# Kernel tuning notes

Measured on AMD Instinct MI355X. Metric: run time of the kernel, lower is better.

The kernel has to match this reference:

```python
import jax, jax.numpy as jnp
import numpy as np

WINDOW = (2, 6, 12)  # (Wz, Wy, Wx)
HEADS = 6


def _position_index(window):
    Wz, Wy, Wx = window
    cz, cy, cx = np.arange(Wz), np.arange(Wy), np.arange(Wx)
    coords = np.stack(np.meshgrid(cz, cy, cx, indexing='ij'))  # [3, Wz, Wy, Wx]
    cf = coords.reshape(3, -1)                                  # [3, N]
    rel = cf[:, :, None] - cf[:, None, :]                       # [3, N, N]
    rel = rel.transpose(1, 2, 0).astype(np.int64)               # [N, N, 3]
    rel[:, :, 0] += Wz - 1
    rel[:, :, 1] += Wy - 1
    rel[:, :, 2] += Wx - 1
    rel[:, :, 0] *= 2 * Wy - 1
    return jnp.asarray(rel.sum(-1).reshape(-1))                 # [N*N]


def setup_inputs() -> dict:
    key = jax.random.key(0)
    ks = jax.random.split(key, 7)
    dim, N, B_, nW = 192, 144, 1024, 512
    table_rows = (2 * WINDOW[2] - 1) * (2 * WINDOW[1] - 1) * (2 * WINDOW[0] - 1)  # 759
    return {
        'x': jax.random.normal(ks[0], (B_, N, dim), jnp.float32),
        'mask': jax.random.normal(ks[1], (nW, N, N), jnp.float32),
        'w_qkv': jax.random.normal(ks[2], (dim, 3 * dim), jnp.float32) * 0.02,
        'b_qkv': jax.random.normal(ks[3], (3 * dim,), jnp.float32) * 0.02,
        'w_o': jax.random.normal(ks[4], (dim, dim), jnp.float32) * 0.02,
        'b_o': jax.random.normal(ks[5], (dim,), jnp.float32) * 0.02,
        'bias_table': jax.random.normal(ks[6], (table_rows, 1, HEADS), jnp.float32) * 0.02,
    }


def reference(x, mask, w_qkv, b_qkv, w_o, b_o, bias_table):
    B_, N, dim = x.shape
    H = HEADS
    hd = dim // H
    scale = hd ** -0.5

    qkv = x @ w_qkv + b_qkv                              # [B_, N, 3*dim]
    qkv = qkv.reshape(B_, N, 3, H, hd).transpose(2, 0, 3, 1, 4)
    q, k, v = qkv[0], qkv[1], qkv[2]                     # [B_, H, N, hd]

    attn = jnp.einsum('bhnd,bhmd->bhnm', q * scale, k)   # [B_, H, N, N]

    pos_idx = _position_index(WINDOW)                    # [N*N] int constant
    bias = bias_table[pos_idx].reshape(N, N, H).transpose(2, 0, 1)  # [H, N, N]
    attn = attn + bias[None]

    nW = mask.shape[0]
    attn = attn.reshape(B_ // nW, nW, H, N, N) + mask[None, :, None]
    attn = jax.nn.softmax(attn.reshape(B_, H, N, N), axis=-1)

    out = jnp.einsum('bhnm,bhmd->bhnd', attn, v)         # [B_, H, N, hd]
    out = out.transpose(0, 2, 1, 3).reshape(B_, N, dim)
    return out @ w_o + b_o
```

## Files before the change

### kernel.cpp

```cpp
#include <hip/hip_runtime.h>

typedef __attribute__((ext_vector_type(4))) float  f32x4;
typedef __attribute__((ext_vector_type(4))) float  float4v;
typedef __attribute__((ext_vector_type(4))) short  short4v;
typedef __attribute__((ext_vector_type(8))) short  short8v;
typedef __attribute__((ext_vector_type(2))) unsigned uint2v;
typedef __attribute__((ext_vector_type(8))) __bf16 bf16x8;

union Frag { short4v h[2]; short8v s8; unsigned u[4]; };
union BF4  { uint2v u2; short4v s4; };

__device__ __forceinline__ short f2bf(float f) {
  unsigned u = __builtin_bit_cast(unsigned, f);
  u = (u + 0x7fffu + ((u >> 16) & 1u)) >> 16;
  return (short)u;
}

__device__ __forceinline__ unsigned cvt_pk_bf16(float a, float b) {
  unsigned r;
  asm("v_cvt_pk_bf16_f32 %0, %1, %2" : "=v"(r) : "v"(a), "v"(b));
  return r;
}
__device__ __forceinline__ short4v f4_to_bf4(float4v v) {
  BF4 r;
  r.u2 = uint2v{ cvt_pk_bf16(v[0], v[1]), cvt_pk_bf16(v[2], v[3]) };
  return r.s4;
}

__device__ __forceinline__ f32x4 mfma_bf16(const Frag& a, const Frag& b, f32x4 c) {
  return __builtin_amdgcn_mfma_f32_16x16x32_bf16(
      __builtin_bit_cast(bf16x8, a.s8), __builtin_bit_cast(bf16x8, b.s8), c, 0, 0, 0);
}

__device__ __forceinline__ int poscode(int i) {
  int z = (i >= 72) ? 1 : 0;
  int rem = i - 72 * z;
  int y = rem / 12;
  return 11 * z + y + (rem - 12 * y);
}

__device__ __forceinline__ int kperm(int r) {
  return (r & 16) ? (((r - 16) >> 2) * 8 + 4 + (r & 3)) : ((r >> 2) * 8 + (r & 3));
}

__global__ __launch_bounds__(256) void k_transpose_w(
    const float* __restrict__ w_qkv, const float* __restrict__ w_o,
    short* __restrict__ wtq, short* __restrict__ wto) {
  int idx = blockIdx.x * 256 + threadIdx.x;
  if (idx < 110592) {
    int k = idx / 576, c = idx % 576;
    int kp = (k & ~31) + kperm(k & 31);
    wtq[c * 192 + kp] = f2bf(w_qkv[idx]);
  } else {
    int j = idx - 110592;
    int k = j / 192, c = j % 192;
    wto[c * 192 + k] = f2bf(w_o[j]);
  }
}

__global__ __launch_bounds__(256) void k_bias(
    const float* __restrict__ btab, float* __restrict__ bias6) {
  int idx = blockIdx.x * 256 + threadIdx.x;
  if (idx >= 124416) return;
  int h = idx / 20736, r = idx % 20736, m = r / 144, n = r % 144;
  bias6[idx] = btab[(poscode(m) - poscode(n) + 27) * 6 + h];
}

__global__ __launch_bounds__(256, 2) void k_qkv(
    const float* __restrict__ x, const float* __restrict__ bqkv,
    const short* __restrict__ wtq, short* __restrict__ qkv) {
  __shared__ short a_lds[128][200];
  __shared__ short bT[288][40];
  const int tid = threadIdx.x;
  const int lane = tid & 63, wv = tid >> 6;
  const int l15 = lane & 15, lg = lane >> 4;

  const int did = blockIdx.x;
  const int vid = (did & 7) * 288 + (did >> 3);
  const int row0 = (vid >> 1) * 128;
  const int col0 = (vid & 1) * 288;

#pragma unroll
  for (int i = 0; i < 24; ++i) {
    int flat = tid + 256 * i;
    int r = flat / 48, c4 = flat % 48;
    float4v xv = *(const float4v*)&x[(size_t)(row0 + r) * 192 + c4 * 4];
    int k = c4 * 4, rr = k & 31;
    int pos = (k & ~31) + ((rr & 16) ? (((rr - 16) >> 2) * 8 + 4) : ((rr >> 2) * 8));
    *(short4v*)&a_lds[r][pos] = f4_to_bf4(xv);
  }

  f32x4 acc[2][18];
#pragma unroll
  for (int ai = 0; ai < 2; ++ai)
#pragma unroll
    for (int i = 0; i < 18; ++i) acc[ai][i] = f32x4{0.f, 0.f, 0.f, 0.f};

  for (int kc = 0; kc < 6; ++kc) {
    __syncthreads();
#pragma unroll
    for (int i = 0; i < 5; ++i) {
      int flat = tid + 256 * i;
      if (flat < 1152) {
        int c = flat >> 2, j = flat & 3;
        *(short8v*)&bT[c][j * 8] =
            *(const short8v*)&wtq[(col0 + c) * 192 + kc * 32 + j * 8];
      }
    }
    __syncthreads();
    Frag a0, a1;
    a0.s8 = *(const short8v*)&a_lds[wv * 32 + l15][kc * 32 + lg * 8];
    a1.s8 = *(const short8v*)&a_lds[wv * 32 + 16 + l15][kc * 32 + lg * 8];
#pragma unroll
    for (int cf = 0; cf < 18; ++cf) {
      Frag bw;
      bw.s8 = *(const short8v*)&bT[cf * 16 + l15][lg * 8];
      acc[0][cf] = mfma_bf16(bw, a0, acc[0][cf]);
      acc[1][cf] = mfma_bf16(bw, a1, acc[1][cf]);
    }
  }

#pragma unroll
  for (int ai = 0; ai < 2; ++ai) {
    const int g = row0 + wv * 32 + ai * 16 + l15;
    const int b_ = g / 144, n = g - b_ * 144;
#pragma unroll
    for (int cf = 0; cf < 18; ++cf) {
      int c0 = col0 + cf * 16 + lg * 4;
      int part = c0 / 192, rem = c0 % 192;
      int h = rem >> 5, d0 = rem & 31;
      int q4 = d0 >> 2;
      int dd0 = (part == 2) ? d0 : ((q4 < 4) ? q4 * 8 : (q4 - 4) * 8 + 4);
      float4v bias4 = *(const float4v*)&bqkv[c0];
      float scale = (part == 0) ? 0.17677669529663687f : 1.0f;
      float4v t = (acc[ai][cf] + bias4) * scale;
      *(short4v*)&qkv[(size_t)((part * 1024 + b_) * 6 + h) * 4608 + n * 32 + dd0] =
          f4_to_bf4(t);
    }
  }
}

__global__ __launch_bounds__(512, 4) void k_attn(
    const short* __restrict__ qkv, const float* __restrict__ mask,
    const float* __restrict__ bias6, float* __restrict__ out) {
  __shared__ short k_l[3][144][40];
  __shared__ short vt[3][32][168];
  const int tid = threadIdx.x;
  const int lane = tid & 63, wv = tid >> 6;
  const int l15 = lane & 15, lg = lane >> 4;

  const int did = blockIdx.x;
  const int vid = (did & 7) * 256 + (did >> 3);
  const int wm = vid >> 2, r4 = vid & 3;
  const int b = wm + (r4 >> 1) * 512;
  const int h0 = (r4 & 1) * 3;

  const size_t kbase = (size_t)((1024 + b) * 6 + h0) * 4608;
#pragma unroll
  for (int i = 0; i < 4; ++i) {
    int flat = tid + 512 * i;
    if (flat < 1728) {
      int h = flat / 576, r = flat % 576;
      int n = r >> 2, j8 = (r & 3) * 8;
      *(short8v*)&k_l[h][n][j8] =
          *(const short8v*)&qkv[kbase + (size_t)h * 4608 + n * 32 + j8];
    }
  }
#pragma unroll
  for (int i = 0; i < 3; ++i) {
    int flat = tid + 512 * i;
    int h = flat / 512, r = flat & 511;
    int d = r >> 4, jj = r & 15;
    vt[h][d][128 + (jj >> 2) * 8 + 4 + (jj & 3)] = 0;
  }
  const size_t vbase = (size_t)((2048 + b) * 6 + h0) * 4608;
#pragma unroll
  for (int i = 0; i < 7; ++i) {
    int flat = tid + 512 * i;
    if (flat < 3456) {
      int h = flat / 1152, r = flat % 1152;
      int n = r >> 3, d4 = (r & 7) * 4;
      short4v vv = *(const short4v*)&qkv[vbase + (size_t)h * 4608 + n * 32 + d4];
      int np = (n & ~31) + kperm(n & 31);
      vt[h][d4 + 0][np] = vv[0];
      vt[h][d4 + 1][np] = vv[1];
      vt[h][d4 + 2][np] = vv[2];
      vt[h][d4 + 3][np] = vv[3];
    }
  }
  __syncthreads();

  const float* maskw = &mask[(size_t)wm * 20736];
  const size_t qb = (size_t)(b * 6 + h0) * 4608;

  f32x4 mrow[9];
  int q = 0;
  for (int unit = 0; unit < 4; ++unit) {
    int t, hl;
    if (unit < 3) { t = wv; hl = unit; }
    else { if (wv >= 3) break; t = 8; hl = wv; }
    if (unit == 0 || unit == 3) {
      q = t * 16 + l15;
#pragma unroll
      for (int cf = 0; cf < 9; ++cf)
        mrow[cf] = *(const float4v*)&maskw[q * 144 + cf * 16 + lg * 4];
    }

    Frag aq;
    aq.s8 = *(const short8v*)&qkv[qb + (size_t)hl * 4608 + q * 32 + lg * 8];

    f32x4 s[9];
#pragma unroll
    for (int cf = 0; cf < 9; ++cf) {
      Frag bk;
      bk.s8 = *(const short8v*)&k_l[hl][cf * 16 + l15][lg * 8];
      s[cf] = mfma_bf16(bk, aq, f32x4{0.f, 0.f, 0.f, 0.f});
    }
    const float* brow = &bias6[(size_t)((h0 + hl) * 144 + q) * 144];
#pragma unroll
    for (int cf = 0; cf < 9; ++cf) {
      float4v bv = *(const float4v*)&brow[cf * 16 + lg * 4];
      s[cf] += mrow[cf] + bv;
    }

    float mx = s[0][0];
#pragma unroll
    for (int cf = 0; cf < 9; ++cf)
#pragma unroll
      for (int reg = 0; reg < 4; ++reg) mx = fmaxf(mx, s[cf][reg]);
    mx = fmaxf(mx, __shfl_xor(mx, 16, 64));
    mx = fmaxf(mx, __shfl_xor(mx, 32, 64));
    float sum = 0.f;
#pragma unroll
    for (int cf = 0; cf < 9; ++cf)
#pragma unroll
      for (int reg = 0; reg < 4; ++reg) {
        float e = __expf(s[cf][reg] - mx);
        s[cf][reg] = e;
        sum += e;
      }
    sum += __shfl_xor(sum, 16, 64);
    sum += __shfl_xor(sum, 32, 64);
    const float rinv = 1.0f / sum;

    f32x4 o0 = {0.f, 0.f, 0.f, 0.f}, o1 = {0.f, 0.f, 0.f, 0.f};
#pragma unroll
    for (int kc = 0; kc < 5; ++kc) {
      Frag p, b0, b1;
      p.u[0] = cvt_pk_bf16(s[2 * kc][0], s[2 * kc][1]);
      p.u[1] = cvt_pk_bf16(s[2 * kc][2], s[2 * kc][3]);
      if (kc < 4) {
        p.u[2] = cvt_pk_bf16(s[2 * kc + 1][0], s[2 * kc + 1][1]);
        p.u[3] = cvt_pk_bf16(s[2 * kc + 1][2], s[2 * kc + 1][3]);
      } else {
        p.u[2] = 0; p.u[3] = 0;
      }
      b0.s8 = *(const short8v*)&vt[hl][l15][kc * 32 + lg * 8];
      b1.s8 = *(const short8v*)&vt[hl][16 + l15][kc * 32 + lg * 8];
      o0 = mfma_bf16(b0, p, o0);
      o1 = mfma_bf16(b1, p, o1);
    }
    o0 *= rinv;
    o1 *= rinv;
    const size_t base = (size_t)(b * 144 + q) * 192 + (h0 + hl) * 32;
    *(float4v*)&out[base + lg * 4]      = o0;
    *(float4v*)&out[base + 16 + lg * 4] = o1;
  }
}

__global__ __launch_bounds__(256, 2) void k_oproj(
    float* __restrict__ io, const float* __restrict__ bo,
    const short* __restrict__ wto) {
  __shared__ short a_lds[64][200];
  __shared__ short bT[192][40];
  const int tid = threadIdx.x;
  const int lane = tid & 63, wv = tid >> 6;
  const int l15 = lane & 15, lg = lane >> 4;
  const int row0 = blockIdx.x * 64;

#pragma unroll
  for (int i = 0; i < 12; ++i) {
    int flat = tid + 256 * i;
    int r = flat / 48, c4 = flat % 48;
    float4v xv = *(const float4v*)&io[(size_t)(row0 + r) * 192 + c4 * 4];
    *(short4v*)&a_lds[r][c4 * 4] = f4_to_bf4(xv);
  }

  f32x4 acc[12];
#pragma unroll
  for (int i = 0; i < 12; ++i) acc[i] = f32x4{0.f, 0.f, 0.f, 0.f};

  for (int kc = 0; kc < 6; ++kc) {
    __syncthreads();
#pragma unroll
    for (int i = 0; i < 6; ++i) {
      int flat = tid + 256 * i;
      int c = flat >> 3, kk = (flat & 7) << 2;
      *(short4v*)&bT[c][kk] = *(const short4v*)&wto[c * 192 + kc * 32 + kk];
    }
    __syncthreads();
    Frag a;
    a.h[0] = *(const short4v*)&a_lds[wv * 16 + l15][kc * 32 + lg * 4];
    a.h[1] = *(const short4v*)&a_lds[wv * 16 + l15][kc * 32 + lg * 4 + 16];
#pragma unroll
    for (int cf = 0; cf < 12; ++cf) {
      Frag bw;
      bw.h[0] = *(const short4v*)&bT[cf * 16 + l15][lg * 4];
      bw.h[1] = *(const short4v*)&bT[cf * 16 + l15][lg * 4 + 16];
      acc[cf] = mfma_bf16(bw, a, acc[cf]);
    }
  }

  const int g = row0 + wv * 16 + l15;
#pragma unroll
  for (int cf = 0; cf < 12; ++cf) {
    int c0 = cf * 16 + lg * 4;
    float4v bias4 = *(const float4v*)&bo[c0];
    *(float4v*)&io[(size_t)g * 192 + c0] = acc[cf] + bias4;
  }
}

extern "C" void kernel_launch(void* const* d_in, const int* in_sizes, int n_in,
                              void* d_out, int out_size, void* d_ws, size_t ws_size,
                              hipStream_t stream) {
  const float* x    = (const float*)d_in[0];
  const float* mask = (const float*)d_in[1];
  const float* wqkv = (const float*)d_in[2];
  const float* bqkv = (const float*)d_in[3];
  const float* wo   = (const float*)d_in[4];
  const float* bo   = (const float*)d_in[5];
  const float* btab = (const float*)d_in[6];
  float* out = (float*)d_out;

  short* wtq   = (short*)d_ws;
  short* wto   = wtq + 110592;
  short* qkv   = wto + 36864;
  float* bias6 = (float*)(qkv + 84934656);

  k_transpose_w<<<576, 256, 0, stream>>>(wqkv, wo, wtq, wto);
  k_bias<<<486, 256, 0, stream>>>(btab, bias6);
  k_qkv<<<2304, 256, 0, stream>>>(x, bqkv, wtq, qkv);
  k_attn<<<2048, 512, 0, stream>>>(qkv, mask, bias6, out);
  k_oproj<<<2304, 256, 0, stream>>>(out, bo, wto);
}
```

Before: 312.3 us.

## Retile QKV GEMM to full-width 64-row blocks with register-prefetched weights

The QKV projection kernel now gives each block 64 rows and all 576 output columns, so x is converted once per row and the column split is gone. The next weight k-slice is loaded into registers while the current one is multiplied, which overlaps global loads with MFMA work and removes one barrier per step. The attention kernel's launch bound drops from 4 to 2 blocks per multiprocessor. This trades fewer wave-level A-fragment reuses (one 16-row fragment per wave instead of two) and a larger LDS footprint and register count for less redundant loading. The blocks-per-SM change on the attention kernel gives the compiler more registers but may reduce occupancy.

```diff
diff --git a/kernel.cpp b/kernel.cpp
--- a/kernel.cpp
+++ b/kernel.cpp
@@ -69,19 +69,22 @@
 __global__ __launch_bounds__(256, 2) void k_qkv(
     const float* __restrict__ x, const float* __restrict__ bqkv,
     const short* __restrict__ wtq, short* __restrict__ qkv) {
-  __shared__ short a_lds[128][200];
-  __shared__ short bT[288][40];
+  __shared__ short a_lds[64][200];
+  __shared__ short bT[576][40];
   const int tid = threadIdx.x;
   const int lane = tid & 63, wv = tid >> 6;
   const int l15 = lane & 15, lg = lane >> 4;
-
-  const int did = blockIdx.x;
-  const int vid = (did & 7) * 288 + (did >> 3);
-  const int row0 = (vid >> 1) * 128;
-  const int col0 = (vid & 1) * 288;
-
-#pragma unroll
-  for (int i = 0; i < 24; ++i) {
+  const int row0 = blockIdx.x * 64;
+  const int bc0 = tid >> 2;
+  const int bj8 = (tid & 3) * 8;
+
+  short8v bpre[9];
+#pragma unroll
+  for (int i = 0; i < 9; ++i)
+    bpre[i] = *(const short8v*)&wtq[(bc0 + 64 * i) * 192 + bj8];
+
+#pragma unroll
+  for (int i = 0; i < 12; ++i) {
     int flat = tid + 256 * i;
     int r = flat / 48, c4 = flat % 48;
     float4v xv = *(const float4v*)&x[(size_t)(row0 + r) * 192 + c4 * 4];
@@ -89,58 +92,56 @@
     int pos = (k & ~31) + ((rr & 16) ? (((rr - 16) >> 2) * 8 + 4) : ((rr >> 2) * 8));
     *(short4v*)&a_lds[r][pos] = f4_to_bf4(xv);
   }
-
-  f32x4 acc[2][18];
-#pragma unroll
-  for (int ai = 0; ai < 2; ++ai)
-#pragma unroll
-    for (int i = 0; i < 18; ++i) acc[ai][i] = f32x4{0.f, 0.f, 0.f, 0.f};
+#pragma unroll
+  for (int i = 0; i < 9; ++i)
+    *(short8v*)&bT[bc0 + 64 * i][bj8] = bpre[i];
+  __syncthreads();
+
+  f32x4 acc[36];
+#pragma unroll
+  for (int i = 0; i < 36; ++i) acc[i] = f32x4{0.f, 0.f, 0.f, 0.f};
 
   for (int kc = 0; kc < 6; ++kc) {
-    __syncthreads();
-#pragma unroll
-    for (int i = 0; i < 5; ++i) {
-      int flat = tid + 256 * i;
-      if (flat < 1152) {
-        int c = flat >> 2, j = flat & 3;
-        *(short8v*)&bT[c][j * 8] =
-            *(const short8v*)&wtq[(col0 + c) * 192 + kc * 32 + j * 8];
-      }
-    }
-    __syncthreads();
-    Frag a0, a1;
-    a0.s8 = *(const short8v*)&a_lds[wv * 32 + l15][kc * 32 + lg * 8];
-    a1.s8 = *(const short8v*)&a_lds[wv * 32 + 16 + l15][kc * 32 + lg * 8];
-#pragma unroll
-    for (int cf = 0; cf < 18; ++cf) {
+    if (kc < 5) {
+#pragma unroll
+      for (int i = 0; i < 9; ++i)
+        bpre[i] = *(const short8v*)&wtq[(bc0 + 64 * i) * 192 + (kc + 1) * 32 + bj8];
+    }
+    Frag a;
+    a.s8 = *(const short8v*)&a_lds[wv * 16 + l15][kc * 32 + lg * 8];
+#pragma unroll
+    for (int cf = 0; cf < 36; ++cf) {
       Frag bw;
       bw.s8 = *(const short8v*)&bT[cf * 16 + l15][lg * 8];
-      acc[0][cf] = mfma_bf16(bw, a0, acc[0][cf]);
-      acc[1][cf] = mfma_bf16(bw, a1, acc[1][cf]);
-    }
-  }
-
-#pragma unroll
-  for (int ai = 0; ai < 2; ++ai) {
-    const int g = row0 + wv * 32 + ai * 16 + l15;
-    const int b_ = g / 144, n = g - b_ * 144;
-#pragma unroll
-    for (int cf = 0; cf < 18; ++cf) {
-      int c0 = col0 + cf * 16 + lg * 4;
-      int part = c0 / 192, rem = c0 % 192;
-      int h = rem >> 5, d0 = rem & 31;
-      int q4 = d0 >> 2;
-      int dd0 = (part == 2) ? d0 : ((q4 < 4) ? q4 * 8 : (q4 - 4) * 8 + 4);
-      float4v bias4 = *(const float4v*)&bqkv[c0];
-      float scale = (part == 0) ? 0.17677669529663687f : 1.0f;
-      float4v t = (acc[ai][cf] + bias4) * scale;
-      *(short4v*)&qkv[(size_t)((part * 1024 + b_) * 6 + h) * 4608 + n * 32 + dd0] =
-          f4_to_bf4(t);
-    }
-  }
-}
-
-__global__ __launch_bounds__(512, 4) void k_attn(
+      acc[cf] = mfma_bf16(bw, a, acc[cf]);
+    }
+    __syncthreads();
+    if (kc < 5) {
+#pragma unroll
+      for (int i = 0; i < 9; ++i)
+        *(short8v*)&bT[bc0 + 64 * i][bj8] = bpre[i];
+      __syncthreads();
+    }
+  }
+
+  const int g = row0 + wv * 16 + l15;
+  const int b_ = g / 144, n = g - b_ * 144;
+#pragma unroll
+  for (int cf = 0; cf < 36; ++cf) {
+    int c0 = cf * 16 + lg * 4;
+    int part = c0 / 192, rem = c0 % 192;
+    int h = rem >> 5, d0 = rem & 31;
+    int q4 = d0 >> 2;
+    int dd0 = (part == 2) ? d0 : ((q4 < 4) ? q4 * 8 : (q4 - 4) * 8 + 4);
+    float4v bias4 = *(const float4v*)&bqkv[c0];
+    float scale = (part == 0) ? 0.17677669529663687f : 1.0f;
+    float4v t = (acc[cf] + bias4) * scale;
+    *(short4v*)&qkv[(size_t)((part * 1024 + b_) * 6 + h) * 4608 + n * 32 + dd0] =
+        f4_to_bf4(t);
+  }
+}
+
+__global__ __launch_bounds__(512, 2) void k_attn(
     const short* __restrict__ qkv, const float* __restrict__ mask,
     const float* __restrict__ bias6, float* __restrict__ out) {
   __shared__ short k_l[3][144][40];
```

After: 283.5 us. 1.1x faster.

## Fuse QKV projection into attention kernel, one block per window

Applied to the files above, without the earlier changes.

Merges the QKV projection GEMM and the attention kernel into one kernel. Each 576-thread block handles one window with all six heads: each wave computes Q/K/V for its 16 rows straight from x, keeps Q in registers and writes K and the transposed V into LDS. This removes the write and re-read of the large bf16 qkv intermediate in global memory and one kernel launch. In exchange, weight fragments are read from global/L2 with no LDS staging, LDS use per block doubles, and register pressure is high (x fragments plus six Q fragments), which may lower occupancy.

```diff
diff --git a/kernel.cpp b/kernel.cpp
--- a/kernel.cpp
+++ b/kernel.cpp
@@ -49,8 +49,7 @@
   int idx = blockIdx.x * 256 + threadIdx.x;
   if (idx < 110592) {
     int k = idx / 576, c = idx % 576;
-    int kp = (k & ~31) + kperm(k & 31);
-    wtq[c * 192 + kp] = f2bf(w_qkv[idx]);
+    wtq[c * 192 + (k & ~31) + kperm(k & 31)] = f2bf(w_qkv[idx]);
   } else {
     int j = idx - 110592;
     int k = j / 192, c = j % 192;
@@ -66,157 +65,95 @@
   bias6[idx] = btab[(poscode(m) - poscode(n) + 27) * 6 + h];
 }
 
-__global__ __launch_bounds__(256, 2) void k_qkv(
+__global__ __launch_bounds__(576, 3) void k_fused(
     const float* __restrict__ x, const float* __restrict__ bqkv,
-    const short* __restrict__ wtq, short* __restrict__ qkv) {
-  __shared__ short a_lds[128][200];
-  __shared__ short bT[288][40];
+    const short* __restrict__ wtq, const float* __restrict__ mask,
+    const float* __restrict__ bias6, float* __restrict__ out) {
+  __shared__ short k_l[6][144][40];
+  __shared__ short vt[6][32][168];
+
   const int tid = threadIdx.x;
   const int lane = tid & 63, wv = tid >> 6;
   const int l15 = lane & 15, lg = lane >> 4;
 
   const int did = blockIdx.x;
-  const int vid = (did & 7) * 288 + (did >> 3);
-  const int row0 = (vid >> 1) * 128;
-  const int col0 = (vid & 1) * 288;
-
-#pragma unroll
-  for (int i = 0; i < 24; ++i) {
-    int flat = tid + 256 * i;
-    int r = flat / 48, c4 = flat % 48;
-    float4v xv = *(const float4v*)&x[(size_t)(row0 + r) * 192 + c4 * 4];
-    int k = c4 * 4, rr = k & 31;
-    int pos = (k & ~31) + ((rr & 16) ? (((rr - 16) >> 2) * 8 + 4) : ((rr >> 2) * 8));
-    *(short4v*)&a_lds[r][pos] = f4_to_bf4(xv);
-  }
-
-  f32x4 acc[2][18];
-#pragma unroll
-  for (int ai = 0; ai < 2; ++ai)
-#pragma unroll
-    for (int i = 0; i < 18; ++i) acc[ai][i] = f32x4{0.f, 0.f, 0.f, 0.f};
-
+  const int vid = (did & 7) * 128 + (did >> 3);
+  const int b = (vid >> 1) + (vid & 1) * 512;
+  const int wm = vid >> 1;
+  const int row = wv * 16 + l15;
+
+  const float* xrow = &x[(size_t)(b * 144 + row) * 192];
+  Frag ax[6];
+#pragma unroll
   for (int kc = 0; kc < 6; ++kc) {
-    __syncthreads();
-#pragma unroll
-    for (int i = 0; i < 5; ++i) {
-      int flat = tid + 256 * i;
-      if (flat < 1152) {
-        int c = flat >> 2, j = flat & 3;
-        *(short8v*)&bT[c][j * 8] =
-            *(const short8v*)&wtq[(col0 + c) * 192 + kc * 32 + j * 8];
-      }
-    }
-    __syncthreads();
-    Frag a0, a1;
-    a0.s8 = *(const short8v*)&a_lds[wv * 32 + l15][kc * 32 + lg * 8];
-    a1.s8 = *(const short8v*)&a_lds[wv * 32 + 16 + l15][kc * 32 + lg * 8];
-#pragma unroll
-    for (int cf = 0; cf < 18; ++cf) {
+    float4v x0 = *(const float4v*)&xrow[kc * 32 + lg * 4];
+    float4v x1 = *(const float4v*)&xrow[kc * 32 + 16 + lg * 4];
+    ax[kc].h[0] = f4_to_bf4(x0);
+    ax[kc].h[1] = f4_to_bf4(x1);
+  }
+
+#pragma unroll
+  for (int i = 0; i < 6; ++i) {
+    int flat = tid + 576 * i;
+    if (flat < 3072) {
+      int h = flat >> 9, r = flat & 511;
+      int d = r >> 4, jj = r & 15;
+      vt[h][d][128 + (jj >> 2) * 8 + 4 + (jj & 3)] = 0;
+    }
+  }
+
+  Frag aq[6];
+  f32x4 qc0;
+#pragma unroll
+  for (int pt = 0; pt < 36; ++pt) {
+    const int part = pt / 12, r12 = pt % 12, hl = r12 >> 1, cc = r12 & 1;
+    const int c0 = part * 192 + hl * 32 + cc * 16;
+    f32x4 acc = {0.f, 0.f, 0.f, 0.f};
+#pragma unroll
+    for (int kc = 0; kc < 6; ++kc) {
       Frag bw;
-      bw.s8 = *(const short8v*)&bT[cf * 16 + l15][lg * 8];
-      acc[0][cf] = mfma_bf16(bw, a0, acc[0][cf]);
-      acc[1][cf] = mfma_bf16(bw, a1, acc[1][cf]);
-    }
-  }
-
-#pragma unroll
-  for (int ai = 0; ai < 2; ++ai) {
-    const int g = row0 + wv * 32 + ai * 16 + l15;
-    const int b_ = g / 144, n = g - b_ * 144;
-#pragma unroll
-    for (int cf = 0; cf < 18; ++cf) {
-      int c0 = col0 + cf * 16 + lg * 4;
-      int part = c0 / 192, rem = c0 % 192;
-      int h = rem >> 5, d0 = rem & 31;
-      int q4 = d0 >> 2;
-      int dd0 = (part == 2) ? d0 : ((q4 < 4) ? q4 * 8 : (q4 - 4) * 8 + 4);
-      float4v bias4 = *(const float4v*)&bqkv[c0];
-      float scale = (part == 0) ? 0.17677669529663687f : 1.0f;
-      float4v t = (acc[ai][cf] + bias4) * scale;
-      *(short4v*)&qkv[(size_t)((part * 1024 + b_) * 6 + h) * 4608 + n * 32 + dd0] =
-          f4_to_bf4(t);
-    }
-  }
-}
-
-__global__ __launch_bounds__(512, 4) void k_attn(
-    const short* __restrict__ qkv, const float* __restrict__ mask,
-    const float* __restrict__ bias6, float* __restrict__ out) {
-  __shared__ short k_l[3][144][40];
-  __shared__ short vt[3][32][168];
-  const int tid = threadIdx.x;
-  const int lane = tid & 63, wv = tid >> 6;
-  const int l15 = lane & 15, lg = lane >> 4;
-
-  const int did = blockIdx.x;
-  const int vid = (did & 7) * 256 + (did >> 3);
-  const int wm = vid >> 2, r4 = vid & 3;
-  const int b = wm + (r4 >> 1) * 512;
-  const int h0 = (r4 & 1) * 3;
-
-  const size_t kbase = (size_t)((1024 + b) * 6 + h0) * 4608;
-#pragma unroll
-  for (int i = 0; i < 4; ++i) {
-    int flat = tid + 512 * i;
-    if (flat < 1728) {
-      int h = flat / 576, r = flat % 576;
-      int n = r >> 2, j8 = (r & 3) * 8;
-      *(short8v*)&k_l[h][n][j8] =
-          *(const short8v*)&qkv[kbase + (size_t)h * 4608 + n * 32 + j8];
-    }
-  }
-#pragma unroll
-  for (int i = 0; i < 3; ++i) {
-    int flat = tid + 512 * i;
-    int h = flat / 512, r = flat & 511;
-    int d = r >> 4, jj = r & 15;
-    vt[h][d][128 + (jj >> 2) * 8 + 4 + (jj & 3)] = 0;
-  }
-  const size_t vbase = (size_t)((2048 + b) * 6 + h0) * 4608;
-#pragma unroll
-  for (int i = 0; i < 7; ++i) {
-    int flat = tid + 512 * i;
-    if (flat < 3456) {
-      int h = flat / 1152, r = flat % 1152;
-      int n = r >> 3, d4 = (r & 7) * 4;
-      short4v vv = *(const short4v*)&qkv[vbase + (size_t)h * 4608 + n * 32 + d4];
-      int np = (n & ~31) + kperm(n & 31);
-      vt[h][d4 + 0][np] = vv[0];
-      vt[h][d4 + 1][np] = vv[1];
-      vt[h][d4 + 2][np] = vv[2];
-      vt[h][d4 + 3][np] = vv[3];
+      bw.s8 = *(const short8v*)&wtq[(c0 + l15) * 192 + kc * 32 + lg * 8];
+      acc = mfma_bf16(bw, ax[kc], acc);
+    }
+    float4v bias4 = *(const float4v*)&bqkv[c0 + lg * 4];
+    if (part == 0) {
+      f32x4 t = (acc + bias4) * 0.17677669529663687f;
+      if (cc == 0) qc0 = t;
+      else { aq[hl].h[0] = f4_to_bf4(qc0); aq[hl].h[1] = f4_to_bf4(t); }
+    } else if (part == 1) {
+      short4v sv = f4_to_bf4(acc + bias4);
+      int d0 = cc * 16 + lg * 4, q4 = d0 >> 2;
+      int dd0 = (q4 < 4) ? q4 * 8 : (q4 - 4) * 8 + 4;
+      *(short4v*)&k_l[hl][row][dd0] = sv;
+    } else {
+      short4v sv = f4_to_bf4(acc + bias4);
+      int np = (row & ~31) + kperm(row & 31);
+      int d0 = cc * 16 + lg * 4;
+      vt[hl][d0 + 0][np] = sv[0];
+      vt[hl][d0 + 1][np] = sv[1];
+      vt[hl][d0 + 2][np] = sv[2];
+      vt[hl][d0 + 3][np] = sv[3];
     }
   }
   __syncthreads();
 
-  const float* maskw = &mask[(size_t)wm * 20736];
-  const size_t qb = (size_t)(b * 6 + h0) * 4608;
-
+  const int q = row;
+  const float* maskw = &mask[(size_t)wm * 20736 + (size_t)q * 144];
   f32x4 mrow[9];
-  int q = 0;
-  for (int unit = 0; unit < 4; ++unit) {
-    int t, hl;
-    if (unit < 3) { t = wv; hl = unit; }
-    else { if (wv >= 3) break; t = 8; hl = wv; }
-    if (unit == 0 || unit == 3) {
-      q = t * 16 + l15;
-#pragma unroll
-      for (int cf = 0; cf < 9; ++cf)
-        mrow[cf] = *(const float4v*)&maskw[q * 144 + cf * 16 + lg * 4];
-    }
-
-    Frag aq;
-    aq.s8 = *(const short8v*)&qkv[qb + (size_t)hl * 4608 + q * 32 + lg * 8];
-
+#pragma unroll
+  for (int cf = 0; cf < 9; ++cf)
+    mrow[cf] = *(const float4v*)&maskw[cf * 16 + lg * 4];
+
+#pragma unroll
+  for (int hl = 0; hl < 6; ++hl) {
     f32x4 s[9];
 #pragma unroll
     for (int cf = 0; cf < 9; ++cf) {
       Frag bk;
       bk.s8 = *(const short8v*)&k_l[hl][cf * 16 + l15][lg * 8];
-      s[cf] = mfma_bf16(bk, aq, f32x4{0.f, 0.f, 0.f, 0.f});
-    }
-    const float* brow = &bias6[(size_t)((h0 + hl) * 144 + q) * 144];
+      s[cf] = mfma_bf16(bk, aq[hl], f32x4{0.f, 0.f, 0.f, 0.f});
+    }
+    const float* brow = &bias6[(size_t)(hl * 144 + q) * 144];
 #pragma unroll
     for (int cf = 0; cf < 9; ++cf) {
       float4v bv = *(const float4v*)&brow[cf * 16 + lg * 4];
@@ -262,7 +199,7 @@
     }
     o0 *= rinv;
     o1 *= rinv;
-    const size_t base = (size_t)(b * 144 + q) * 192 + (h0 + hl) * 32;
+    const size_t base = (size_t)(b * 144 + q) * 192 + hl * 32;
     *(float4v*)&out[base + lg * 4]      = o0;
     *(float4v*)&out[base + 16 + lg * 4] = o1;
   }
@@ -334,12 +271,10 @@
 
   short* wtq   = (short*)d_ws;
   short* wto   = wtq + 110592;
-  short* qkv   = wto + 36864;
-  float* bias6 = (float*)(qkv + 84934656);
+  float* bias6 = (float*)(wto + 36864);
 
   k_transpose_w<<<576, 256, 0, stream>>>(wqkv, wo, wtq, wto);
   k_bias<<<486, 256, 0, stream>>>(btab, bias6);
-  k_qkv<<<2304, 256, 0, stream>>>(x, bqkv, wtq, qkv);
-  k_attn<<<2048, 512, 0, stream>>>(qkv, mask, bias6, out);
+  k_fused<<<1024, 576, 0, stream>>>(x, bqkv, wtq, mask, bias6, out);
   k_oproj<<<2304, 256, 0, stream>>>(out, bo, wto);
 }
```

Measured after the change: 408.3 us. 1.31x slower.
